# Optimization experiments

Measured on AMD Instinct MI355X. Metric: run time of the kernel, lower is better.

## Reference

```python
import jax, jax.numpy as jnp
import numpy as np

D = 256   # model dim
M = 64    # num mechanisms
B = 4
S = 8192


def setup_inputs() -> dict:
    key = jax.random.key(0)
    ks = jax.random.split(key, 16)
    n = jax.random.normal
    inp = {
        "x": n(ks[0], (B, S, D), jnp.float32),
        "context": n(ks[1], (B, S, D), jnp.float32),
        # stacked per-mechanism params (m, out, in) etc.
        "Wm": n(ks[2], (M, D, D), jnp.float32) * (1.0 / np.sqrt(D)),
        "bm": n(ks[3], (M, D), jnp.float32) * 0.02,
        "cm": n(ks[4], (M, D), jnp.float32),           # characteristics (1,1,dim) per node
        "um": n(ks[5], (M, D), jnp.float32) * (1.0 / np.sqrt(D)),  # timing_gate weight
        "vm": n(ks[6], (M,), jnp.float32) * 0.02,       # timing_gate bias
        # selector: Linear(d, 2d) -> GELU -> Linear(2d, m)
        "W1": n(ks[7], (2 * D, D), jnp.float32) * (1.0 / np.sqrt(D)),
        "b1": n(ks[8], (2 * D,), jnp.float32) * 0.02,
        "W2": n(ks[9], (M, 2 * D), jnp.float32) * (1.0 / np.sqrt(2 * D)),
        "b2": n(ks[10], (M,), jnp.float32) * 0.02,
        # integrate: Linear(2d, d)
        "Wi": n(ks[11], (D, 2 * D), jnp.float32) * (1.0 / np.sqrt(2 * D)),
        "bi": n(ks[12], (D,), jnp.float32) * 0.02,
    }
    return inp


def reference(x, context, Wm, bm, cm, um, vm, W1, b1, W2, b2, Wi, bi):
    # selector: softmax over mechanisms (b, s, m)
    h = jax.nn.gelu(jnp.einsum('bsd,ed->bse', context, W1) + b1, approximate=False)
    scores = jax.nn.softmax(jnp.einsum('bse,me->bsm', h, W2) + b2, axis=-1)

    # per-mechanism sigmoid timing gate (b, s, m)
    gate = jax.nn.sigmoid(jnp.einsum('bsd,md->bsm', x, um) + vm)

    # combined weight a[b,s,m] = softmax_score * gate; then
    # selected = sum_m a * (x @ Wm.T + bm + cm)  -- contracted without
    # materializing the (b, s, m, d) stack the torch loop builds.
    a = scores * gate                               # (b, s, m)
    selected = jnp.einsum('bsm,bse,mde->bsd', a, x, Wm) \
             + jnp.einsum('bsm,md->bsd', a, bm + cm)

    # integrate(concat([x, selected]))
    cat = jnp.concatenate([x, selected], axis=-1)   # (b, s, 2d)
    integrated = jnp.einsum('bse,de->bsd', cat, Wi) + bi
    return integrated
```

## Files before the change

### kernel.cpp

```cpp
#include <hip/hip_runtime.h>
#include <cstdint>
#include <cstddef>


typedef _Float16 f16;
typedef f16 f16x8 __attribute__((ext_vector_type(8)));
typedef float f32x4 __attribute__((ext_vector_type(4)));

#define DEV __device__ __forceinline__

DEV uint32_t swz128(uint32_t b) { return b ^ (((b >> 7) & 7u) << 4); }
DEV uint32_t swz512(uint32_t b) { return b ^ (((b >> 9) & 7u) << 4); }

DEV void gload_lds16(const void* g, void* l) {
  __builtin_amdgcn_global_load_lds(
      (const __attribute__((address_space(1))) unsigned int*)g,
      (__attribute__((address_space(3))) unsigned int*)l, 16, 0, 0);
}

DEV f16x8 cvt8(float4 u0, float4 u1) {
  f16x8 v = {(f16)u0.x, (f16)u0.y, (f16)u0.z, (f16)u0.w,
             (f16)u1.x, (f16)u1.y, (f16)u1.z, (f16)u1.w};
  return v;
}

__global__ void prep_b_kernel(const float* __restrict__ S, f16* __restrict__ dst,
                              int K, int BN, int total) {
  int t = blockIdx.x * 256 + threadIdx.x;
  if (t >= total) return;
  int gpc = BN * 8;
  int g = t % gpc;
  int c = (t / gpc) % (K / 64);
  int cb = t / (gpc * (K / 64));
  int ks = g / (BN * 4);
  int rem = g % (BN * 4);
  int col = rem >> 2;
  int kg = rem & 3;
  int J = cb * BN + col;
  int k = c * 64 + ks * 32 + kg * 8;
  const float* s = S + (size_t)J * K + k;
  float4 u0 = *(const float4*)s;
  float4 u1 = *(const float4*)(s + 4);
  f16* chunk = dst + (size_t)(cb * (K / 64) + c) * (BN * 64);
  *(f16x8*)((char*)chunk + swz128((uint32_t)g * 16)) = cvt8(u0, u1);
}

__global__ void prep_wcat_kernel(const float* __restrict__ Wm,
                                 const float* __restrict__ bm,
                                 const float* __restrict__ cm,
                                 f16* __restrict__ dst) {
  int t = blockIdx.x * 256 + threadIdx.x;
  if (t >= 257 * 2048) return;
  int g = t & 2047;
  int c = t >> 11;
  int ks = g >> 10;
  int rem = g & 1023;
  int col = rem >> 2;
  int kg = rem & 3;
  int k0 = ks * 32 + kg * 8;
  f16x8 v;
  if (c < 256) {
    int m = c >> 2;
    int e0 = (c & 3) * 64 + k0;
    const float* s = Wm + ((size_t)m * 256 + col) * 256 + e0;
    float4 u0 = *(const float4*)s;
    float4 u1 = *(const float4*)(s + 4);
    v = cvt8(u0, u1);
  } else {
#pragma unroll
    for (int j = 0; j < 8; ++j) {
      int k = k0 + j;
      v[j] = (f16)(bm[k * 256 + col] + cm[k * 256 + col]);
    }
  }
  *(f16x8*)((char*)(dst + (size_t)c * 16384) + swz128((uint32_t)g * 16)) = v;
}

template <int BN, int NCHUNK, int A0C, int EPI>
__global__ __launch_bounds__(BN == 256 ? 512 : 256, 2)
void gemm_tpl(const float* __restrict__ A0, int lda0,
              const f16* __restrict__ A1, int lda1,
              const f16* __restrict__ Bt,
              const float* __restrict__ bias,
              float* __restrict__ outF, f16* __restrict__ outH, int ldo) {
  constexpr int WAVES = (BN == 256) ? 8 : 4;
  constexpr int THREADS = WAVES * 64;
  constexpr int WC = (BN == 256) ? 4 : 1;
  constexpr int WR = WAVES / WC;
  constexpr int RT = 128 / (WR * 16);
  constexpr int CT = (BN / WC) / 16;

  __shared__ alignas(16) f16 sA[2][128 * 64];
  __shared__ alignas(16) f16 sB[2][BN * 64];

  const int tid = threadIdx.x;
  const int lane = tid & 63;
  const int wid = tid >> 6;
  const int wr = wid / WC, wc = wid % WC;
  const int rb = blockIdx.x, cb = blockIdx.y;

  auto stageB = [&](int c, int buf) {
    const char* src = (const char*)(Bt + (size_t)(cb * NCHUNK + c) * (BN * 64));
#pragma unroll
    for (int it = 0; it < (BN * 64 * 2) / (THREADS * 16); ++it) {
      int off = (it * THREADS + tid) * 16;
      gload_lds16(src + off, (char*)&sB[buf][0] + off);
    }
  };
  auto stageA = [&](int c, int buf) {
#pragma unroll
    for (int it = 0; it < 1024 / THREADS; ++it) {
      int gg = it * THREADS + tid;
      int row = gg >> 3, eg = gg & 7;
      size_t rowG = (size_t)rb * 128 + row;
      f16x8 v;
      if (A0C > 0 && c < A0C) {
        const float* s = A0 + rowG * lda0 + c * 64 + eg * 8;
        float4 u0 = *(const float4*)s;
        float4 u1 = *(const float4*)(s + 4);
        v = cvt8(u0, u1);
      } else {
        v = *(const f16x8*)(A1 + rowG * lda1 + (c - A0C) * 64 + eg * 8);
      }
      *(f16x8*)((char*)&sA[buf][0] + swz128((uint32_t)(row * 128 + eg * 16))) = v;
    }
  };

  f32x4 acc[RT][CT];
#pragma unroll
  for (int i = 0; i < RT; ++i)
#pragma unroll
    for (int j = 0; j < CT; ++j) acc[i][j] = (f32x4){0.f, 0.f, 0.f, 0.f};

  stageB(0, 0);
  stageA(0, 0);
  __syncthreads();

  for (int c = 0; c < NCHUNK; ++c) {
    int cur = c & 1;
    if (c + 1 < NCHUNK) {
      stageB(c + 1, cur ^ 1);
      stageA(c + 1, cur ^ 1);
    }
#pragma unroll
    for (int ks = 0; ks < 2; ++ks) {
      f16x8 af[RT], bf[CT];
#pragma unroll
      for (int rt = 0; rt < RT; ++rt) {
        int row = wr * (RT * 16) + rt * 16 + (lane & 15);
        af[rt] = *(const f16x8*)((const char*)&sA[cur][0] +
                                 swz128((uint32_t)(row * 128 + ks * 64 + (lane >> 4) * 16)));
      }
#pragma unroll
      for (int ct = 0; ct < CT; ++ct) {
        int col = wc * (CT * 16) + ct * 16 + (lane & 15);
        bf[ct] = *(const f16x8*)((const char*)&sB[cur][0] +
                                 swz128((uint32_t)(((ks * BN + col) * 4 + (lane >> 4)) * 16)));
      }
#pragma unroll
      for (int rt = 0; rt < RT; ++rt)
#pragma unroll
        for (int ct = 0; ct < CT; ++ct)
          acc[rt][ct] = __builtin_amdgcn_mfma_f32_16x16x32_f16(af[rt], bf[ct], acc[rt][ct], 0, 0, 0);
    }
    __syncthreads();
  }

#pragma unroll
  for (int rt = 0; rt < RT; ++rt)
#pragma unroll
    for (int ct = 0; ct < CT; ++ct)
#pragma unroll
      for (int i = 0; i < 4; ++i) {
        size_t row = (size_t)rb * 128 + wr * (RT * 16) + rt * 16 + (lane >> 4) * 4 + i;
        int colG = cb * BN + wc * (CT * 16) + ct * 16 + (lane & 15);
        float v = acc[rt][ct][i];
        if constexpr (EPI == 0) {
          if (bias) v += bias[colG];
          outF[row * ldo + colG] = v;
        } else {
          v += bias[colG];
          float ge = 0.5f * v * (1.0f + erff(v * 0.70710678118f));
          outH[row * ldo + colG] = (f16)ge;
        }
      }
}

__global__ void selector_finish(const float* __restrict__ logits,
                                const float* __restrict__ glog,
                                const float* __restrict__ b2,
                                const float* __restrict__ vm,
                                f16* __restrict__ a16) {
  int n = blockIdx.x * 4 + (threadIdx.x >> 6);
  int m = threadIdx.x & 63;
  float l = logits[(size_t)n * 64 + m] + b2[m];
  float mx = l;
#pragma unroll
  for (int o = 32; o; o >>= 1) mx = fmaxf(mx, __shfl_xor(mx, o));
  float p = expf(l - mx);
  float s = p;
#pragma unroll
  for (int o = 32; o; o >>= 1) s += __shfl_xor(s, o);
  float g = glog[(size_t)n * 64 + m] + vm[m];
  float gate = 1.0f / (1.0f + expf(-g));
  a16[(size_t)n * 64 + m] = (f16)(p / s * gate);
}

__global__ __launch_bounds__(512, 2)
void big_gemm(const float* __restrict__ x, const f16* __restrict__ a16,
              const f16* __restrict__ Wcat, f16* __restrict__ sel) {
  __shared__ alignas(16) f16 sX[128 * 256];
  __shared__ alignas(16) f16 sAa[128 * 72];
  __shared__ alignas(16) f16 sB[2][256 * 64];

  const int tid = threadIdx.x;
  const int lane = tid & 63;
  const int wid = tid >> 6;
  const int wr = wid >> 2, wc = wid & 3;
  const int rb = blockIdx.x;

  auto stageB = [&](int c, int buf) {
    const char* src = (const char*)(Wcat + (size_t)c * 16384);
#pragma unroll
    for (int it = 0; it < 4; ++it) {
      int off = (it * 512 + tid) * 16;
      gload_lds16(src + off, (char*)&sB[buf][0] + off);
    }
  };

#pragma unroll
  for (int it = 0; it < 8; ++it) {
    int gg = it * 512 + tid;
    int row = gg >> 5, eg = gg & 31;
    const float* s = x + ((size_t)rb * 128 + row) * 256 + eg * 8;
    float4 u0 = *(const float4*)s;
    float4 u1 = *(const float4*)(s + 4);
    *(f16x8*)((char*)sX + swz512((uint32_t)(row * 512 + eg * 16))) = cvt8(u0, u1);
  }
#pragma unroll
  for (int it = 0; it < 2; ++it) {
    int gg = it * 512 + tid;
    int row = gg >> 3, mg = gg & 7;
    f16x8 v = *(const f16x8*)(a16 + ((size_t)rb * 128 + row) * 64 + mg * 8);
    *(f16x8*)((char*)sAa + row * 144 + mg * 16) = v;
  }
  stageB(0, 0);
  __syncthreads();

  f32x4 acc[4][4];
#pragma unroll
  for (int i = 0; i < 4; ++i)
#pragma unroll
    for (int j = 0; j < 4; ++j) acc[i][j] = (f32x4){0.f, 0.f, 0.f, 0.f};

  for (int c = 0; c < 257; ++c) {
    int cur = c & 1;
    if (c + 1 < 257) stageB(c + 1, cur ^ 1);
    if (c < 256) {
      int m = c >> 2;
      int ebyte = (c & 3) * 128;
      f16 as[4];
#pragma unroll
      for (int rt = 0; rt < 4; ++rt) {
        int row = wr * 64 + rt * 16 + (lane & 15);
        as[rt] = sAa[row * 72 + m];
      }
#pragma unroll
      for (int ks = 0; ks < 2; ++ks) {
        f16x8 af[4], bf[4];
#pragma unroll
        for (int rt = 0; rt < 4; ++rt) {
          int row = wr * 64 + rt * 16 + (lane & 15);
          f16x8 xv = *(const f16x8*)((const char*)sX +
                       swz512((uint32_t)(row * 512 + ebyte + ks * 64 + (lane >> 4) * 16)));
          af[rt] = xv * as[rt];
        }
#pragma unroll
        for (int ct = 0; ct < 4; ++ct) {
          int col = wc * 64 + ct * 16 + (lane & 15);
          bf[ct] = *(const f16x8*)((const char*)&sB[cur][0] +
                     swz128((uint32_t)(((ks * 256 + col) * 4 + (lane >> 4)) * 16)));
        }
#pragma unroll
        for (int rt = 0; rt < 4; ++rt)
#pragma unroll
          for (int ct = 0; ct < 4; ++ct)
            acc[rt][ct] = __builtin_amdgcn_mfma_f32_16x16x32_f16(af[rt], bf[ct], acc[rt][ct], 0, 0, 0);
      }
    } else {
#pragma unroll
      for (int ks = 0; ks < 2; ++ks) {
        f16x8 af[4], bf[4];
#pragma unroll
        for (int rt = 0; rt < 4; ++rt) {
          int row = wr * 64 + rt * 16 + (lane & 15);
          af[rt] = *(const f16x8*)((const char*)sAa + row * 144 + ks * 64 + (lane >> 4) * 16);
        }
#pragma unroll
        for (int ct = 0; ct < 4; ++ct) {
          int col = wc * 64 + ct * 16 + (lane & 15);
          bf[ct] = *(const f16x8*)((const char*)&sB[cur][0] +
                     swz128((uint32_t)(((ks * 256 + col) * 4 + (lane >> 4)) * 16)));
        }
#pragma unroll
        for (int rt = 0; rt < 4; ++rt)
#pragma unroll
          for (int ct = 0; ct < 4; ++ct)
            acc[rt][ct] = __builtin_amdgcn_mfma_f32_16x16x32_f16(af[rt], bf[ct], acc[rt][ct], 0, 0, 0);
      }
    }
    __syncthreads();
  }

#pragma unroll
  for (int rt = 0; rt < 4; ++rt)
#pragma unroll
    for (int ct = 0; ct < 4; ++ct)
#pragma unroll
      for (int i = 0; i < 4; ++i) {
        size_t row = (size_t)rb * 128 + wr * 64 + rt * 16 + (lane >> 4) * 4 + i;
        int col = wc * 64 + ct * 16 + (lane & 15);
        sel[row * 256 + col] = (f16)acc[rt][ct][i];
      }
}

extern "C" void kernel_launch(void* const* d_in, const int* in_sizes, int n_in,
                              void* d_out, int out_size, void* d_ws, size_t ws_size,
                              hipStream_t stream) {
  (void)in_sizes; (void)n_in; (void)out_size;
  const float* x   = (const float*)d_in[0];
  const float* ctx = (const float*)d_in[1];
  const float* Wm  = (const float*)d_in[2];
  const float* bm  = (const float*)d_in[3];
  const float* cm  = (const float*)d_in[4];
  const float* um  = (const float*)d_in[5];
  const float* vm  = (const float*)d_in[6];
  const float* W1  = (const float*)d_in[7];
  const float* b1  = (const float*)d_in[8];
  const float* W2  = (const float*)d_in[9];
  const float* b2  = (const float*)d_in[10];
  const float* Wi  = (const float*)d_in[11];
  const float* bi  = (const float*)d_in[12];
  float* out = (float*)d_out;

  char* ws = (char*)d_ws;
  size_t off = 0;
  f16* Wcat = (f16*)(ws + off); off += (size_t)257 * 16384 * 2;
  f16* W1t  = (f16*)(ws + off); off += (size_t)512 * 256 * 2;
  f16* W2t  = (f16*)(ws + off); off += (size_t)64 * 512 * 2;
  f16* umt  = (f16*)(ws + off); off += (size_t)64 * 256 * 2;
  f16* Wit  = (f16*)(ws + off); off += (size_t)256 * 512 * 2;
  f16* h16  = (f16*)(ws + off); off += (size_t)32768 * 512 * 2;
  float* logits = (float*)(ws + off); off += (size_t)32768 * 64 * 4;
  float* glog   = (float*)(ws + off); off += (size_t)32768 * 64 * 4;
  f16* a16   = (f16*)(ws + off); off += (size_t)32768 * 64 * 2;
  f16* sel16 = (f16*)(ws + off); off += (size_t)32768 * 256 * 2;
  if (ws_size < off) return;

  prep_wcat_kernel<<<dim3(257 * 2048 / 256), dim3(256), 0, stream>>>(Wm, bm, cm, Wcat);
  prep_b_kernel<<<dim3(16384 / 256), dim3(256), 0, stream>>>(W1, W1t, 256, 256, 16384);
  prep_b_kernel<<<dim3(4096 / 256),  dim3(256), 0, stream>>>(W2, W2t, 512, 64, 4096);
  prep_b_kernel<<<dim3(2048 / 256),  dim3(256), 0, stream>>>(um, umt, 256, 64, 2048);
  prep_b_kernel<<<dim3(16384 / 256), dim3(256), 0, stream>>>(Wi, Wit, 512, 256, 16384);

  gemm_tpl<256, 4, 4, 1><<<dim3(256, 2), dim3(512), 0, stream>>>(
      ctx, 256, nullptr, 0, W1t, b1, nullptr, h16, 512);
  gemm_tpl<64, 4, 4, 0><<<dim3(256, 1), dim3(256), 0, stream>>>(
      x, 256, nullptr, 0, umt, nullptr, glog, nullptr, 64);
  gemm_tpl<64, 8, 0, 0><<<dim3(256, 1), dim3(256), 0, stream>>>(
      nullptr, 0, h16, 512, W2t, nullptr, logits, nullptr, 64);
  selector_finish<<<dim3(32768 / 4), dim3(256), 0, stream>>>(logits, glog, b2, vm, a16);

  big_gemm<<<dim3(256), dim3(512), 0, stream>>>(x, a16, Wcat, sel16);

  gemm_tpl<256, 8, 4, 0><<<dim3(256, 1), dim3(512), 0, stream>>>(
      x, 256, sel16, 256, Wit, bi, out, nullptr, 256);
}
```

Measured before the change: 408.9 us.

## Reorder weight chunks mechanism-inner and keep x fragments in registers across mechanisms

Changes the packed weight layout so chunks iterate over mechanisms in the inner loop and the embedding slice in the outer loop. The x fragments then load from LDS only once every 64 chunks and stay in registers, where before they were reloaded every chunk. The main loop replaces __syncthreads with explicit vmcnt waits and raw barriers, so the next chunk's global-to-LDS load can stay in flight while the current one is consumed. It also adds setprio around the MFMA block and peels the bias chunk out of the loop. The trade-off is higher register pressure from holding the x fragments, and correctness depends on the hand-written vmcnt count matching the number of loads stageB issues.

```diff
diff --git a/kernel.cpp b/kernel.cpp
--- a/kernel.cpp
+++ b/kernel.cpp
@@ -60,8 +60,8 @@
   int k0 = ks * 32 + kg * 8;
   f16x8 v;
   if (c < 256) {
-    int m = c >> 2;
-    int e0 = (c & 3) * 64 + k0;
+    int m = c & 63;
+    int e0 = (c >> 6) * 64 + k0;
     const float* s = Wm + ((size_t)m * 256 + col) * 256 + e0;
     float4 u0 = *(const float4*)s;
     float4 u1 = *(const float4*)(s + 4);
@@ -245,7 +245,8 @@
     *(f16x8*)((char*)sAa + row * 144 + mg * 16) = v;
   }
   stageB(0, 0);
-  __syncthreads();
+  asm volatile("s_waitcnt vmcnt(0) lgkmcnt(0)" ::: "memory");
+  __builtin_amdgcn_s_barrier();
 
   f32x4 acc[4][4];
 #pragma unroll
@@ -253,63 +254,76 @@
 #pragma unroll
     for (int j = 0; j < 4; ++j) acc[i][j] = (f32x4){0.f, 0.f, 0.f, 0.f};
 
-  for (int c = 0; c < 257; ++c) {
-    int cur = c & 1;
-    if (c + 1 < 257) stageB(c + 1, cur ^ 1);
-    if (c < 256) {
-      int m = c >> 2;
-      int ebyte = (c & 3) * 128;
-      f16 as[4];
-#pragma unroll
-      for (int rt = 0; rt < 4; ++rt) {
-        int row = wr * 64 + rt * 16 + (lane & 15);
-        as[rt] = sAa[row * 72 + m];
-      }
-#pragma unroll
-      for (int ks = 0; ks < 2; ++ks) {
-        f16x8 af[4], bf[4];
+  const int row0 = wr * 64 + (lane & 15);
+  f16x8 xv[2][4];
+
+  for (int q = 0; q < 256; ++q) {
+    int cur = q & 1;
+    stageB(q + 1, cur ^ 1);
+    asm volatile("s_waitcnt vmcnt(4)" ::: "memory");
+    __builtin_amdgcn_s_barrier();
+
+    if ((q & 63) == 0) {
+      int ebyte = (q >> 6) * 128;
+#pragma unroll
+      for (int ks = 0; ks < 2; ++ks)
 #pragma unroll
         for (int rt = 0; rt < 4; ++rt) {
-          int row = wr * 64 + rt * 16 + (lane & 15);
-          f16x8 xv = *(const f16x8*)((const char*)sX +
-                       swz512((uint32_t)(row * 512 + ebyte + ks * 64 + (lane >> 4) * 16)));
-          af[rt] = xv * as[rt];
+          int row = row0 + rt * 16;
+          xv[ks][rt] = *(const f16x8*)((const char*)sX +
+              swz512((uint32_t)(row * 512 + ebyte + ks * 64 + (lane >> 4) * 16)));
         }
-#pragma unroll
-        for (int ct = 0; ct < 4; ++ct) {
-          int col = wc * 64 + ct * 16 + (lane & 15);
-          bf[ct] = *(const f16x8*)((const char*)&sB[cur][0] +
-                     swz128((uint32_t)(((ks * 256 + col) * 4 + (lane >> 4)) * 16)));
-        }
-#pragma unroll
-        for (int rt = 0; rt < 4; ++rt)
-#pragma unroll
-          for (int ct = 0; ct < 4; ++ct)
-            acc[rt][ct] = __builtin_amdgcn_mfma_f32_16x16x32_f16(af[rt], bf[ct], acc[rt][ct], 0, 0, 0);
-      }
-    } else {
-#pragma unroll
-      for (int ks = 0; ks < 2; ++ks) {
-        f16x8 af[4], bf[4];
-#pragma unroll
-        for (int rt = 0; rt < 4; ++rt) {
-          int row = wr * 64 + rt * 16 + (lane & 15);
-          af[rt] = *(const f16x8*)((const char*)sAa + row * 144 + ks * 64 + (lane >> 4) * 16);
-        }
-#pragma unroll
-        for (int ct = 0; ct < 4; ++ct) {
-          int col = wc * 64 + ct * 16 + (lane & 15);
-          bf[ct] = *(const f16x8*)((const char*)&sB[cur][0] +
-                     swz128((uint32_t)(((ks * 256 + col) * 4 + (lane >> 4)) * 16)));
-        }
-#pragma unroll
-        for (int rt = 0; rt < 4; ++rt)
-#pragma unroll
-          for (int ct = 0; ct < 4; ++ct)
-            acc[rt][ct] = __builtin_amdgcn_mfma_f32_16x16x32_f16(af[rt], bf[ct], acc[rt][ct], 0, 0, 0);
-      }
-    }
-    __syncthreads();
+    }
+    int m = q & 63;
+    f16 as[4];
+#pragma unroll
+    for (int rt = 0; rt < 4; ++rt) as[rt] = sAa[(row0 + rt * 16) * 72 + m];
+
+#pragma unroll
+    for (int ks = 0; ks < 2; ++ks) {
+      f16x8 bf[4];
+#pragma unroll
+      for (int ct = 0; ct < 4; ++ct) {
+        int col = wc * 64 + ct * 16 + (lane & 15);
+        bf[ct] = *(const f16x8*)((const char*)&sB[cur][0] +
+                   swz128((uint32_t)(((ks * 256 + col) * 4 + (lane >> 4)) * 16)));
+      }
+      f16x8 af[4];
+#pragma unroll
+      for (int rt = 0; rt < 4; ++rt) af[rt] = xv[ks][rt] * as[rt];
+      __builtin_amdgcn_s_setprio(1);
+#pragma unroll
+      for (int rt = 0; rt < 4; ++rt)
+#pragma unroll
+        for (int ct = 0; ct < 4; ++ct)
+          acc[rt][ct] = __builtin_amdgcn_mfma_f32_16x16x32_f16(af[rt], bf[ct], acc[rt][ct], 0, 0, 0);
+      __builtin_amdgcn_s_setprio(0);
+    }
+    __builtin_amdgcn_sched_barrier(0);
+    __builtin_amdgcn_s_barrier();
+  }
+
+  asm volatile("s_waitcnt vmcnt(0)" ::: "memory");
+  __builtin_amdgcn_s_barrier();
+#pragma unroll
+  for (int ks = 0; ks < 2; ++ks) {
+    f16x8 af[4], bf[4];
+#pragma unroll
+    for (int rt = 0; rt < 4; ++rt) {
+      int row = row0 + rt * 16;
+      af[rt] = *(const f16x8*)((const char*)sAa + row * 144 + ks * 64 + (lane >> 4) * 16);
+    }
+#pragma unroll
+    for (int ct = 0; ct < 4; ++ct) {
+      int col = wc * 64 + ct * 16 + (lane & 15);
+      bf[ct] = *(const f16x8*)((const char*)&sB[0][0] +
+                 swz128((uint32_t)(((ks * 256 + col) * 4 + (lane >> 4)) * 16)));
+    }
+#pragma unroll
+    for (int rt = 0; rt < 4; ++rt)
+#pragma unroll
+      for (int ct = 0; ct < 4; ++ct)
+        acc[rt][ct] = __builtin_amdgcn_mfma_f32_16x16x32_f16(af[rt], bf[ct], acc[rt][ct], 0, 0, 0);
   }
 
 #pragma unroll
```

Result: faster. 398.1 us (-2.6%).
